# Kernel optimization log

Measured on AMD Instinct MI355X. Metric: run time of the kernel, lower is better.

The kernel has to match this reference:

```python
import jax, jax.numpy as jnp
import numpy as np

NUM_HEADS = 16
DIM = 1024


def setup_inputs() -> dict:
    key = jax.random.key(0)
    kx, kw, kb = jax.random.split(key, 3)
    x = jax.random.normal(kx, (4, 2048, DIM), dtype=jnp.float32)
    # torch Linear(dim, 3*dim): weight [3d, d], bias [3d]; store as [d, 3d] for x @ W
    W_qkv = jax.random.normal(kw, (DIM, 3 * DIM), dtype=jnp.float32) * (1.0 / np.sqrt(DIM))
    b_qkv = jax.random.normal(kb, (3 * DIM,), dtype=jnp.float32) * 0.01
    return {"x": x, "W_qkv": W_qkv, "b_qkv": b_qkv}


def reference(x, W_qkv, b_qkv):
    b, t, d = x.shape
    h = NUM_HEADS
    hd = d // h
    qkv = x @ W_qkv + b_qkv  # [b, t, 3d]
    q, k, v = jnp.split(qkv, 3, axis=-1)
    # [b, t, h, hd] -> [b, h, t, hd]
    q = q.reshape(b, t, h, hd).transpose(0, 2, 1, 3)
    k = k.reshape(b, t, h, hd).transpose(0, 2, 1, 3)
    v = v.reshape(b, t, h, hd).transpose(0, 2, 1, 3)
    # NOTE: original scales by sqrt(full dim d), not head_dim
    logits = jnp.einsum("bhqc,bhkc->bhqk", q, k) / jnp.sqrt(jnp.float32(d))
    causal = jnp.tril(jnp.ones((t, t), dtype=bool))  # [t, t]
    logits = jnp.where(causal, logits, -jnp.inf)
    attn = jax.nn.softmax(logits, axis=-1)
    out = jnp.einsum("bhqk,bhkc->bhqc", attn, v)  # [b, h, t, hd]
    return out.transpose(0, 2, 1, 3).reshape(b, t, d)
```

## Files before the change

kernel.cpp:

```cpp
#include <hip/hip_runtime.h>
#include <hip/hip_bf16.h>

#define D_MODEL 1024
#define N3      3072
#define TSEQ    2048
#define M_TOT   8192

typedef __bf16 bf16_8 __attribute__((ext_vector_type(8)));
typedef float  f32x4  __attribute__((ext_vector_type(4)));
typedef short  s16x4  __attribute__((ext_vector_type(4)));

static __device__ __forceinline__ unsigned short f2bf(float f) {
  __hip_bfloat16 h = __float2bfloat16(f);
  unsigned short u;
  __builtin_memcpy(&u, &h, 2);
  return u;
}
static __device__ __forceinline__ unsigned pack2(float lo, float hi) {
  return (unsigned)f2bf(lo) | ((unsigned)f2bf(hi) << 16);
}
static __device__ __forceinline__ void gload16(const void* g, void* l) {
  __builtin_amdgcn_global_load_lds((const __attribute__((address_space(1))) void*)g,
                                   (__attribute__((address_space(3))) void*)l, 16, 0, 0);
}

__global__ void cvt_x_kernel(const float* __restrict__ x, __bf16* __restrict__ xb) {
  size_t i = (size_t)blockIdx.x * 256 + threadIdx.x;
  float4 v = *(const float4*)(x + i * 4);
  ushort4 o;
  o.x = f2bf(v.x); o.y = f2bf(v.y); o.z = f2bf(v.z); o.w = f2bf(v.w);
  *(ushort4*)((unsigned short*)xb + i * 4) = o;
}

__global__ void cvt_w_kernel(const float* __restrict__ W, __bf16* __restrict__ WT) {
  __shared__ unsigned short tl[64][68];
  int t = threadIdx.x;
  int n0 = blockIdx.x * 64, k0 = blockIdx.y * 64;
  int rr = t >> 4, cc = (t & 15) * 4;
#pragma unroll
  for (int i = 0; i < 4; ++i) {
    int r = rr + i * 16;
    float4 v = *(const float4*)(W + (size_t)(k0 + r) * N3 + n0 + cc);
    tl[r][cc] = f2bf(v.x); tl[r][cc + 1] = f2bf(v.y);
    tl[r][cc + 2] = f2bf(v.z); tl[r][cc + 3] = f2bf(v.w);
  }
  __syncthreads();
#pragma unroll
  for (int i = 0; i < 4; ++i) {
    int rc = rr + i * 16;
    ushort4 o;
    o.x = tl[cc + 0][rc]; o.y = tl[cc + 1][rc];
    o.z = tl[cc + 2][rc]; o.w = tl[cc + 3][rc];
    *(ushort4*)((unsigned short*)WT + (size_t)(n0 + rc) * D_MODEL + k0 + cc) = o;
  }
}

__global__ __launch_bounds__(256, 2) void gemm_qkv_kernel(
    const __bf16* __restrict__ A, const __bf16* __restrict__ Bt,
    const float* __restrict__ bias, __bf16* __restrict__ C, __bf16* __restrict__ VT) {
  __shared__ __align__(16) __bf16 Al[2][4096];
  __shared__ __align__(16) __bf16 Bl[2][4096];
  int tid = threadIdx.x;
  int wave = tid >> 6, lane = tid & 63;
  int lr = lane & 15, lg = lane >> 4;
  int m0 = blockIdx.x * 128, n0 = blockIdx.y * 128;
  int wm = (wave >> 1) * 64, wn = (wave & 1) * 64;

  const f32x4 fz = {0.f, 0.f, 0.f, 0.f};
  f32x4 acc[4][4];
#pragma unroll
  for (int i = 0; i < 4; ++i)
#pragma unroll
    for (int j = 0; j < 4; ++j) acc[i][j] = fz;

  auto stage = [&](int buf, int kt) {
#pragma unroll
    for (int call = 0; call < 2; ++call) {
      int cb = call * 256 + wave * 64;
      int c = cb + lane;
      int row = c >> 2;
      int cir = (c & 3) ^ ((row >> 1) & 3);
      gload16(A + (size_t)(m0 + row) * D_MODEL + kt * 32 + cir * 8, &Al[buf][cb * 8]);
      gload16(Bt + (size_t)(n0 + row) * D_MODEL + kt * 32 + cir * 8, &Bl[buf][cb * 8]);
    }
  };

  stage(0, 0);
  __syncthreads();
  for (int kt = 0; kt < 32; ++kt) {
    int buf = kt & 1;
    if (kt + 1 < 32) stage(buf ^ 1, kt + 1);
    bf16_8 af[4], bv[4];
#pragma unroll
    for (int mb = 0; mb < 4; ++mb) {
      int row = wm + mb * 16 + lr;
      int cir = lg ^ ((row >> 1) & 3);
      af[mb] = *(const bf16_8*)&Al[buf][row * 32 + cir * 8];
    }
#pragma unroll
    for (int nb = 0; nb < 4; ++nb) {
      int row = wn + nb * 16 + lr;
      int cir = lg ^ ((row >> 1) & 3);
      bv[nb] = *(const bf16_8*)&Bl[buf][row * 32 + cir * 8];
    }
#pragma unroll
    for (int mb = 0; mb < 4; ++mb)
#pragma unroll
      for (int nb = 0; nb < 4; ++nb)
        acc[mb][nb] = __builtin_amdgcn_mfma_f32_16x16x32_bf16(af[mb], bv[nb], acc[mb][nb], 0, 0, 0);
    __syncthreads();
  }

  float bvs[4];
#pragma unroll
  for (int nb = 0; nb < 4; ++nb) bvs[nb] = bias[n0 + wn + nb * 16 + lr];

  if (n0 < 2048) {
    const float SC = 0.04508422f;
    float oscale = (n0 < 1024) ? SC : 1.0f;
    unsigned short* C16 = (unsigned short*)C;
#pragma unroll
    for (int mb = 0; mb < 4; ++mb)
#pragma unroll
      for (int nb = 0; nb < 4; ++nb)
#pragma unroll
        for (int r = 0; r < 4; ++r) {
          int row = m0 + wm + mb * 16 + lg * 4 + r;
          int col = n0 + wn + nb * 16 + lr;
          C16[(size_t)row * N3 + col] = f2bf((acc[mb][nb][r] + bvs[nb]) * oscale);
        }
  } else {
    unsigned short* VT16 = (unsigned short*)VT;
#pragma unroll
    for (int mb = 0; mb < 4; ++mb)
#pragma unroll
      for (int nb = 0; nb < 4; ++nb) {
        int row = m0 + wm + mb * 16 + lg * 4;
        int b_ = row >> 11, t = row & 2047;
        int cg = n0 - 2048 + wn + nb * 16 + lr;
        int h_ = cg >> 6, c_ = cg & 63;
        ushort4 o;
        o.x = f2bf(acc[mb][nb][0] + bvs[nb]);
        o.y = f2bf(acc[mb][nb][1] + bvs[nb]);
        o.z = f2bf(acc[mb][nb][2] + bvs[nb]);
        o.w = f2bf(acc[mb][nb][3] + bvs[nb]);
        *(ushort4*)(VT16 + ((size_t)((b_ * 16 + h_) * 64 + c_) * TSEQ + t)) = o;
      }
  }
}

__global__ __launch_bounds__(256, 2) void attn_kernel(
    const __bf16* __restrict__ qkv, const __bf16* __restrict__ VT,
    float* __restrict__ out) {
  __shared__ __align__(16) char smem[32768];

  int lin = blockIdx.x;
  int y = lin & 63;
  int qt = 15 - (lin >> 6);
  int bh = (y & 7) * 8 + (y >> 3);
  int b = bh >> 4, h = bh & 15;
  int tid = threadIdx.x, wave = tid >> 6, lane = tid & 63;
  int lr = lane & 15, lg = lane >> 4;
  int q0 = qt * 128 + wave * 32;

  const __bf16* Kg = qkv + (size_t)b * TSEQ * N3 + 1024 + h * 64;
  const __bf16* Vg = VT + (size_t)bh * 64 * TSEQ;

  auto stage = [&](int buf, int kv0) {
    __bf16* Kl = (__bf16*)(smem + buf * 16384);
    __bf16* Vl = (__bf16*)(smem + buf * 16384 + 8192);
#pragma unroll
    for (int call = 0; call < 2; ++call) {
      int cb = call * 256 + wave * 64;
      int c = cb + lane;
      int row = c >> 3;
      int cir = (c & 7) ^ (row & 7);
      gload16(Kg + (size_t)(kv0 + row) * N3 + cir * 8, Kl + cb * 8);
      gload16(Vg + (size_t)row * TSEQ + kv0 + cir * 8, Vl + cb * 8);
    }
  };

  bf16_8 qf[2][2];
#pragma unroll
  for (int nb = 0; nb < 2; ++nb)
#pragma unroll
    for (int kk = 0; kk < 2; ++kk)
      qf[nb][kk] = *(const bf16_8*)&qkv[(size_t)(b * TSEQ + q0 + nb * 16 + lr) * N3 + h * 64 + kk * 32 + lg * 8];

  float ps[2] = {0.f, 0.f};
  const f32x4 fz = {0.f, 0.f, 0.f, 0.f};
  f32x4 oacc[4][2];
#pragma unroll
  for (int i = 0; i < 4; ++i) { oacc[i][0] = fz; oacc[i][1] = fz; }

  int ntiles = (qt + 1) * 2;
  stage(0, 0);
  asm volatile("s_waitcnt vmcnt(0)" ::: "memory");
  __builtin_amdgcn_sched_barrier(0);
  __builtin_amdgcn_s_barrier();

  for (int tt = 0; tt < ntiles; ++tt) {
    int cur = tt & 1;
    if (tt + 1 < ntiles) stage(cur ^ 1, (tt + 1) * 64);
    __builtin_amdgcn_sched_barrier(0);

    int kv0 = tt * 64;
    if (kv0 <= q0 + 31) {
      const __bf16* Kb = (const __bf16*)(smem + cur * 16384);
      const __bf16* Vb = (const __bf16*)(smem + cur * 16384 + 8192);
      f32x4 st[4][2];
#pragma unroll
      for (int i = 0; i < 4; ++i) { st[i][0] = fz; st[i][1] = fz; }
#pragma unroll
      for (int kk = 0; kk < 2; ++kk) {
        bf16_8 kf[4];
#pragma unroll
        for (int mb = 0; mb < 4; ++mb) {
          int row = mb * 16 + lr;
          int cir = (kk * 4 + lg) ^ (row & 7);
          kf[mb] = *(const bf16_8*)&Kb[row * 64 + cir * 8];
        }
        __builtin_amdgcn_s_setprio(1);
#pragma unroll
        for (int mb = 0; mb < 4; ++mb)
#pragma unroll
          for (int nb = 0; nb < 2; ++nb)
            st[mb][nb] = __builtin_amdgcn_mfma_f32_16x16x32_bf16(kf[mb], qf[nb][kk], st[mb][nb], 0, 0, 0);
        __builtin_amdgcn_s_setprio(0);
      }
      unsigned pw[4][2][2];
      if (kv0 + 63 > q0) {
#pragma unroll
        for (int mb = 0; mb < 4; ++mb)
#pragma unroll
          for (int nb = 0; nb < 2; ++nb) {
            float p[4];
            int qq = q0 + nb * 16 + lr;
#pragma unroll
            for (int r = 0; r < 4; ++r) {
              int kv = kv0 + mb * 16 + lg * 4 + r;
              float s = (kv > qq) ? -1e30f : st[mb][nb][r];
              p[r] = __builtin_amdgcn_exp2f(s);
              ps[nb] += p[r];
            }
            pw[mb][nb][0] = pack2(p[0], p[1]);
            pw[mb][nb][1] = pack2(p[2], p[3]);
          }
      } else {
#pragma unroll
        for (int mb = 0; mb < 4; ++mb)
#pragma unroll
          for (int nb = 0; nb < 2; ++nb) {
            float p[4];
#pragma unroll
            for (int r = 0; r < 4; ++r) {
              p[r] = __builtin_amdgcn_exp2f(st[mb][nb][r]);
              ps[nb] += p[r];
            }
            pw[mb][nb][0] = pack2(p[0], p[1]);
            pw[mb][nb][1] = pack2(p[2], p[3]);
          }
      }
#pragma unroll
      for (int mb = 0; mb < 4; ++mb) {
        s16x4 vf[4];
        int chunk = mb * 2 + (lg >> 1);
#pragma unroll
        for (int mbc = 0; mbc < 4; ++mbc) {
          int row = mbc * 16 + lr;
          int cir = chunk ^ (row & 7);
          vf[mbc] = *(const s16x4*)((const char*)Vb + row * 128 + cir * 16 + (lg & 1) * 8);
        }
        __builtin_amdgcn_s_setprio(1);
#pragma unroll
        for (int nb = 0; nb < 2; ++nb) {
          union { unsigned u[2]; s16x4 v; } pf;
          pf.u[0] = pw[mb][nb][0];
          pf.u[1] = pw[mb][nb][1];
#pragma unroll
          for (int mbc = 0; mbc < 4; ++mbc)
            oacc[mbc][nb] = __builtin_amdgcn_mfma_f32_16x16x16bf16_1k(vf[mbc], pf.v, oacc[mbc][nb], 0, 0, 0);
        }
        __builtin_amdgcn_s_setprio(0);
      }
    }

    if (tt + 1 < ntiles) {
      asm volatile("s_waitcnt vmcnt(0)" ::: "memory");
      __builtin_amdgcn_sched_barrier(0);
      __builtin_amdgcn_s_barrier();
    }
  }

#pragma unroll
  for (int nb = 0; nb < 2; ++nb) {
    float s = ps[nb];
    s += __shfl_xor(s, 16, 64);
    s += __shfl_xor(s, 32, 64);
    float invl = 1.f / s;
    float* dst = out + (size_t)(b * TSEQ + q0 + nb * 16 + lr) * D_MODEL + h * 64 + lg * 4;
#pragma unroll
    for (int mbc = 0; mbc < 4; ++mbc) {
      float4 v;
      v.x = oacc[mbc][nb][0] * invl; v.y = oacc[mbc][nb][1] * invl;
      v.z = oacc[mbc][nb][2] * invl; v.w = oacc[mbc][nb][3] * invl;
      *(float4*)(dst + mbc * 16) = v;
    }
  }
}

extern "C" void kernel_launch(void* const* d_in, const int* in_sizes, int n_in,
                              void* d_out, int out_size, void* d_ws, size_t ws_size,
                              hipStream_t stream) {
  const float* x = (const float*)d_in[0];
  const float* W = (const float*)d_in[1];
  const float* bias = (const float*)d_in[2];
  float* out = (float*)d_out;
  char* ws = (char*)d_ws;
  __bf16* xb  = (__bf16*)(ws);
  __bf16* WT  = (__bf16*)(ws + (size_t)16777216);
  __bf16* qkv = (__bf16*)(ws + (size_t)23068672);
  __bf16* VT  = (__bf16*)(ws + (size_t)73400320);

  hipLaunchKernelGGL(cvt_x_kernel, dim3(8192), dim3(256), 0, stream, x, xb);
  hipLaunchKernelGGL(cvt_w_kernel, dim3(48, 16), dim3(256), 0, stream, W, WT);
  hipLaunchKernelGGL(gemm_qkv_kernel, dim3(64, 24), dim3(256), 0, stream, xb, WT, bias, qkv, VT);
  hipLaunchKernelGGL(attn_kernel, dim3(1024), dim3(256), 0, stream, qkv, VT, out);
}
```

Before: 130.4 us.

## Triple-buffer QKV GEMM LDS staging with partial vmcnt waits and MFMA priority

Moves the QKV projection GEMM from double to triple buffering in shared memory. Loads are issued two K-steps ahead, and each iteration waits only on the older group with s_waitcnt vmcnt(4) plus a raw s_barrier, replacing the full __syncthreads drain. The MFMA block is also wrapped in s_setprio. Together these aim to hide global load latency better, at the cost of 48KB LDS per block, which may limit occupancy to the 2 blocks per CU the launch bounds request.

```diff
diff --git a/kernel.cpp b/kernel.cpp
--- a/kernel.cpp
+++ b/kernel.cpp
@@ -58,8 +58,7 @@
 __global__ __launch_bounds__(256, 2) void gemm_qkv_kernel(
     const __bf16* __restrict__ A, const __bf16* __restrict__ Bt,
     const float* __restrict__ bias, __bf16* __restrict__ C, __bf16* __restrict__ VT) {
-  __shared__ __align__(16) __bf16 Al[2][4096];
-  __shared__ __align__(16) __bf16 Bl[2][4096];
+  __shared__ __align__(16) char smem[49152];
   int tid = threadIdx.x;
   int wave = tid >> 6, lane = tid & 63;
   int lr = lane & 15, lg = lane >> 4;
@@ -74,41 +73,58 @@
     for (int j = 0; j < 4; ++j) acc[i][j] = fz;
 
   auto stage = [&](int buf, int kt) {
+    __bf16* Al = (__bf16*)(smem + buf * 16384);
+    __bf16* Bl = (__bf16*)(smem + buf * 16384 + 8192);
 #pragma unroll
     for (int call = 0; call < 2; ++call) {
       int cb = call * 256 + wave * 64;
       int c = cb + lane;
       int row = c >> 2;
       int cir = (c & 3) ^ ((row >> 1) & 3);
-      gload16(A + (size_t)(m0 + row) * D_MODEL + kt * 32 + cir * 8, &Al[buf][cb * 8]);
-      gload16(Bt + (size_t)(n0 + row) * D_MODEL + kt * 32 + cir * 8, &Bl[buf][cb * 8]);
+      gload16(A + (size_t)(m0 + row) * D_MODEL + kt * 32 + cir * 8, Al + cb * 8);
+      gload16(Bt + (size_t)(n0 + row) * D_MODEL + kt * 32 + cir * 8, Bl + cb * 8);
     }
   };
 
-  stage(0, 0);
-  __syncthreads();
+  stage(0, 0); stage(1, 1);
+  asm volatile("s_waitcnt vmcnt(4)" ::: "memory");
+  __builtin_amdgcn_sched_barrier(0);
+  __builtin_amdgcn_s_barrier();
+
+  int cur = 0;
   for (int kt = 0; kt < 32; ++kt) {
-    int buf = kt & 1;
-    if (kt + 1 < 32) stage(buf ^ 1, kt + 1);
+    if (kt + 2 < 32) stage(cur == 0 ? 2 : cur - 1, kt + 2);
+
+    const __bf16* Al = (const __bf16*)(smem + cur * 16384);
+    const __bf16* Bl = (const __bf16*)(smem + cur * 16384 + 8192);
     bf16_8 af[4], bv[4];
 #pragma unroll
     for (int mb = 0; mb < 4; ++mb) {
       int row = wm + mb * 16 + lr;
       int cir = lg ^ ((row >> 1) & 3);
-      af[mb] = *(const bf16_8*)&Al[buf][row * 32 + cir * 8];
+      af[mb] = *(const bf16_8*)&Al[row * 32 + cir * 8];
     }
 #pragma unroll
     for (int nb = 0; nb < 4; ++nb) {
       int row = wn + nb * 16 + lr;
       int cir = lg ^ ((row >> 1) & 3);
-      bv[nb] = *(const bf16_8*)&Bl[buf][row * 32 + cir * 8];
-    }
+      bv[nb] = *(const bf16_8*)&Bl[row * 32 + cir * 8];
+    }
+    __builtin_amdgcn_s_setprio(1);
 #pragma unroll
     for (int mb = 0; mb < 4; ++mb)
 #pragma unroll
       for (int nb = 0; nb < 4; ++nb)
         acc[mb][nb] = __builtin_amdgcn_mfma_f32_16x16x32_bf16(af[mb], bv[nb], acc[mb][nb], 0, 0, 0);
-    __syncthreads();
+    __builtin_amdgcn_s_setprio(0);
+
+    if (kt + 1 < 32) {
+      if (kt + 2 < 32) asm volatile("s_waitcnt vmcnt(4)" ::: "memory");
+      else             asm volatile("s_waitcnt vmcnt(0)" ::: "memory");
+      __builtin_amdgcn_sched_barrier(0);
+      __builtin_amdgcn_s_barrier();
+    }
+    cur = (cur == 2) ? 0 : cur + 1;
   }
 
   float bvs[4];
```

Result: no change. 131.1 us (+0.6%).
